# Kernel optimization log

Hardware: AMD Instinct MI355X
Metric: run time of the kernel (lower is better)

The kernel has to match this reference:

```python
import jax, jax.numpy as jnp
import numpy as np

B, S, V = 16, 512, 100000
DE, DT, DI = 100, 20, 20      # word / entity-type / entity-id embed dims
H = 128                        # lstm hidden per direction
GD = 2 * H                     # gcn_dim = 256
ITERS = 2
BANK = GD * (ITERS + 1)        # 768
N, E, P, R = 128, 48, 512, 97  # nodes, entities, h-t pairs, relations
CLS = BANK * 2 + 20            # rel_embed size with distance embedding
IN = DE + DT + DI              # encoder input size


def setup_inputs() -> dict:
    key = jax.random.key(0)
    ks = jax.random.split(key, 24)
    words = jax.random.randint(ks[0], (B, S), 0, V, dtype=jnp.int32)
    src_lengths = jax.random.randint(ks[1], (B,), S // 2, S + 1, dtype=jnp.int32)
    mask = (jnp.arange(S)[None, :] < src_lengths[:, None]).astype(jnp.int32)
    entity_type = jax.random.randint(ks[2], (B, S), 0, 7, dtype=jnp.int32)
    entity_id = jax.random.randint(ks[3], (B, S), 0, 81, dtype=jnp.int32)
    # graph_info: [start, end, entity_id, node_type]; spans inside the doc
    starts = jnp.sort(jax.random.randint(ks[4], (B, N), 0, S - 9, dtype=jnp.int32), axis=-1)
    spans = jax.random.randint(ks[5], (B, N), 1, 9, dtype=jnp.int32)
    eids = jax.random.randint(ks[6], (B, N), 0, E, dtype=jnp.int32)
    ntype = jnp.where(jnp.arange(N)[None, :] < 96, 2, 1).astype(jnp.int32) * jnp.ones((B, 1), jnp.int32)
    graph_info = jnp.stack([starts, starts + spans, eids, ntype], axis=-1)
    graph_node_num = jax.random.randint(ks[7], (B,), N // 2, N + 1, dtype=jnp.int32)
    graph_adj = jax.random.randint(ks[8], (B, N, N), 0, 5, dtype=jnp.int32)
    h_t_pairs = jax.random.randint(ks[9], (B, P, 2), 0, E, dtype=jnp.int32)
    ht_pair_distance = jax.random.randint(ks[10], (B, P), 0, 20, dtype=jnp.int32)
    sc = 0.02
    word_table = jax.random.normal(ks[11], (V, DE), jnp.float32) * sc
    word_table = word_table.at[0].set(0.0)  # padding_idx
    type_table = jax.random.normal(ks[12], (7, DT), jnp.float32) * sc
    id_table = jax.random.normal(ks[13], (81, DI), jnp.float32) * sc
    Wih_f = jax.random.normal(ks[14], (4 * H, IN), jnp.float32) * sc
    Whh_f = jax.random.normal(ks[15], (4 * H, H), jnp.float32) * sc
    b_f = jnp.zeros((4 * H,), jnp.float32)
    Wih_b = jax.random.normal(ks[16], (4 * H, IN), jnp.float32) * sc
    Whh_b = jax.random.normal(ks[17], (4 * H, H), jnp.float32) * sc
    b_b = jnp.zeros((4 * H,), jnp.float32)
    gcn_W1 = jax.random.normal(ks[18], (GD, GD), jnp.float32) * sc
    gcn_b1 = jnp.zeros((GD,), jnp.float32)
    gcn_W2 = jax.random.normal(ks[19], (GD, GD), jnp.float32) * sc
    gcn_b2 = jnp.zeros((GD,), jnp.float32)
    dis_table = jax.random.normal(ks[20], (20, 20), jnp.float32) * sc
    pW1 = jax.random.normal(ks[21], (CLS, BANK * 2), jnp.float32) * sc
    pb1 = jnp.zeros((BANK * 2,), jnp.float32)
    pW2 = jax.random.normal(ks[22], (BANK * 2, R), jnp.float32) * sc
    pb2 = jnp.zeros((R,), jnp.float32)
    return dict(words=words, mask=mask, entity_type=entity_type, entity_id=entity_id,
                src_lengths=src_lengths, graph_adj=graph_adj, graph_info=graph_info,
                graph_node_num=graph_node_num, h_t_pairs=h_t_pairs,
                ht_pair_distance=ht_pair_distance,
                word_table=word_table, type_table=type_table, id_table=id_table,
                Wih_f=Wih_f, Whh_f=Whh_f, b_f=b_f, Wih_b=Wih_b, Whh_b=Whh_b, b_b=b_b,
                gcn_W1=gcn_W1, gcn_b1=gcn_b1, gcn_W2=gcn_W2, gcn_b2=gcn_b2,
                dis_table=dis_table, pW1=pW1, pb1=pb1, pW2=pW2, pb2=pb2)


def _lstm(x, Wih, Whh, b, reverse):
    # x: [S, B, IN] -> hs: [S, B, H]
    Bsz = x.shape[1]
    h0 = jnp.zeros((Bsz, H), x.dtype)
    c0 = jnp.zeros((Bsz, H), x.dtype)
    def step(carry, xt):
        h, c = carry
        g = xt @ Wih.T + h @ Whh.T + b
        i, f, gg, o = jnp.split(g, 4, axis=-1)
        c = jax.nn.sigmoid(f) * c + jax.nn.sigmoid(i) * jnp.tanh(gg)
        h = jax.nn.sigmoid(o) * jnp.tanh(c)
        return (h, c), h
    _, hs = jax.lax.scan(step, (h0, c0), x, reverse=reverse)
    return hs


def _forward(words, mask, entity_type, entity_id, src_lengths, graph_adj, graph_info,
             graph_node_num, h_t_pairs, ht_pair_distance,
             word_table, type_table, id_table, Wih_f, Whh_f, b_f, Wih_b, Whh_b, b_b,
             gcn_W1, gcn_b1, gcn_W2, gcn_b2, dis_table, pW1, pb1, pW2, pb2):
    # --- embeddings + BiLSTM encoder ---
    src = jnp.concatenate([word_table[words], type_table[entity_type], id_table[entity_id]], axis=-1)
    xs = jnp.transpose(src, (1, 0, 2))  # [S,B,IN]
    hf = _lstm(xs, Wih_f, Whh_f, b_f, reverse=False)
    hb = _lstm(xs, Wih_b, Whh_b, b_b, reverse=True)
    enc = jnp.transpose(jnp.concatenate([hf, hb], -1), (1, 0, 2))  # [B,S,GD]
    enc = enc * mask[..., None].astype(enc.dtype)  # encoder_outputs[mask==0]=0
    # --- vectorized mergy_span_token: mean of tokens in [start,end) via cumsum ---
    cs = jnp.concatenate([jnp.zeros((enc.shape[0], 1, GD), enc.dtype), jnp.cumsum(enc, axis=1)], axis=1)
    st, en = graph_info[..., 0], graph_info[..., 1]
    span_sum = (jnp.take_along_axis(cs, en[..., None], axis=1)
                - jnp.take_along_axis(cs, st[..., None], axis=1))
    span_len = jnp.maximum(en - st, 1).astype(enc.dtype)[..., None]
    node_mask = (jnp.arange(N)[None, :] < graph_node_num[:, None])
    graph_fea = span_sum / span_len * node_mask[..., None].astype(enc.dtype)  # [B,N,GD]
    # --- GraphReasonLayer (gcn, 2 iters, dense-concat) ---
    A = ((graph_adj > 0) & node_mask[:, :, None] & node_mask[:, None, :]).astype(enc.dtype)
    Anorm = A / jnp.maximum(A.sum(-1, keepdims=True), 1.0)
    h1 = jnp.maximum(jnp.einsum('bmn,bnd->bmd', Anorm, graph_fea) @ gcn_W1 + gcn_b1, 0.0)
    h2 = jnp.maximum(jnp.einsum('bmn,bnd->bmd', Anorm, h1) @ gcn_W2 + gcn_b2, 0.0)
    feat = jnp.concatenate([graph_fea, h1, h2], axis=-1)  # [B,N,BANK]
    # --- entity bank: mean of mention nodes per entity (vectorized select matrix) ---
    m_mask = (graph_info[..., 3] == 2) & node_mask
    sel = ((graph_info[..., 2][:, None, :] == jnp.arange(E)[None, :, None]) & m_mask[:, None, :]).astype(enc.dtype)
    sel = sel / jnp.maximum(sel.sum(-1, keepdims=True), 1.0)
    entity_bank = jnp.einsum('ben,bnd->bed', sel, feat)  # [B,E,BANK]
    # --- head/tail gather + distance embedding + predict MLP ---
    h_ent = jnp.take_along_axis(entity_bank, h_t_pairs[..., 0][..., None], axis=1)
    t_ent = jnp.take_along_axis(entity_bank, h_t_pairs[..., 1][..., None], axis=1)
    rel = jnp.concatenate([h_ent, t_ent, dis_table[ht_pair_distance]], axis=-1)  # [B,P,CLS]
    scores = jnp.tanh(rel @ pW1 + pb1) @ pW2 + pb2  # [B,P,R]
    return scores


def reference(words, mask, entity_type, entity_id, src_lengths, graph_adj, graph_info,
              graph_node_num, h_t_pairs, ht_pair_distance,
              word_table, type_table, id_table, Wih_f, Whh_f, b_f, Wih_b, Whh_b, b_b,
              gcn_W1, gcn_b1, gcn_W2, gcn_b2, dis_table, pW1, pb1, pW2, pb2):
    return _forward(words, mask, entity_type, entity_id, src_lengths, graph_adj, graph_info,
                    graph_node_num, h_t_pairs, ht_pair_distance,
                    word_table, type_table, id_table, Wih_f, Whh_f, b_f, Wih_b, Whh_b, b_b,
                    gcn_W1, gcn_b1, gcn_W2, gcn_b2, dis_table, pW1, pb1, pW2, pb2)
```

## Files before the change

### kernel.cpp

```cpp
#include <hip/hip_runtime.h>
#include <math.h>

static constexpr int B_ = 16, S_ = 512, H_ = 128, G4_ = 512, IN_ = 140;
static constexpr int GD_ = 256, N_ = 128, E_ = 48, P_ = 512, R_ = 97;
static constexpr int BANK_ = 768, UC_ = 1536;

__device__ __forceinline__ float sigf(float x) { return 1.0f / (1.0f + expf(-x)); }

__global__ void transpose_w(const float* __restrict__ Wf, const float* __restrict__ Wb,
                            float* __restrict__ WfT, float* __restrict__ WbT) {
    int i = blockIdx.x * 256 + threadIdx.x;
    if (i < G4_ * IN_) {
        int j = i / IN_, k = i % IN_;
        WfT[k * G4_ + j] = Wf[i];
        WbT[k * G4_ + j] = Wb[i];
    }
}

__global__ __launch_bounds__(512) void embed_xpre(
    const int* __restrict__ words, const int* __restrict__ etype, const int* __restrict__ eidm,
    const float* __restrict__ wt, const float* __restrict__ tt, const float* __restrict__ it,
    const float* __restrict__ WfT, const float* __restrict__ WbT,
    const float* __restrict__ bf, const float* __restrict__ bb,
    float* __restrict__ xf, float* __restrict__ xb) {
    __shared__ float xl[16][IN_];
    int tid = threadIdx.x;
    int r0 = blockIdx.x * 16;
    for (int r = 0; r < 16; ++r) {
        int rid = r0 + r, s = rid >> 4, b = rid & 15;
        if (tid < IN_) {
            int k = tid; float v;
            if (k < 100)      { int w  = words[b * S_ + s]; v = wt[w * 100 + k]; }
            else if (k < 120) { int ty = etype[b * S_ + s]; v = tt[ty * 20 + (k - 100)]; }
            else              { int id = eidm[b * S_ + s];  v = it[id * 20 + (k - 120)]; }
            xl[r][k] = v;
        }
    }
    __syncthreads();
    int j = tid;
    float accf[16], accb[16];
    float bfv = bf[j], bbv = bb[j];
#pragma unroll
    for (int r = 0; r < 16; ++r) { accf[r] = bfv; accb[r] = bbv; }
#pragma unroll 4
    for (int k = 0; k < IN_; ++k) {
        float wf = WfT[k * G4_ + j], wb = WbT[k * G4_ + j];
#pragma unroll
        for (int r = 0; r < 16; ++r) {
            float x = xl[r][k];
            accf[r] += x * wf;
            accb[r] += x * wb;
        }
    }
#pragma unroll
    for (int r = 0; r < 16; ++r) {
        int rid = r0 + r;
        xf[rid * G4_ + j] = accf[r];
        xb[rid * G4_ + j] = accb[r];
    }
}

__global__ __launch_bounds__(512, 1) void lstm_kernel(
    const float* __restrict__ xf, const float* __restrict__ xb,
    const float* __restrict__ Whf, const float* __restrict__ Whb,
    float* __restrict__ hf, float* __restrict__ hb) {
    int bid = blockIdx.x;
    int dir = bid >> 4, b = bid & 15;
    const float* xpre = dir ? xb : xf;
    const float* Whh  = dir ? Whb : Whf;
    float* outp       = dir ? hb : hf;
    int tid  = threadIdx.x;
    int wave = tid >> 6;
    int lane = tid & 63;
    int j4   = lane & 15;
    int ks   = lane >> 4;
    int j    = wave * 16 + j4;

    float4 w4[4][8];
#pragma unroll
    for (int g = 0; g < 4; ++g)
#pragma unroll
        for (int q = 0; q < 8; ++q)
            w4[g][q] = *reinterpret_cast<const float4*>(
                &Whh[(j + 128 * g) * 128 + 32 * ks + 4 * q]);

    __shared__ float hsh[2][128];
    if (tid < 128) { hsh[0][tid] = 0.0f; hsh[1][tid] = 0.0f; }
    float c = 0.0f;

    int t0 = dir ? (S_ - 1) : 0;
    const float* xr0 = &xpre[(t0 * B_ + b) * G4_];
    float xi = xr0[j], xfv = xr0[j + 128], xg = xr0[j + 256], xo = xr0[j + 384];
    __syncthreads();

    for (int t = 0; t < S_; ++t) {
        int tcur = dir ? (S_ - 1 - t) : t;
        float cxi = xi, cxf = xfv, cxg = xg, cxo = xo;
        if (t < S_ - 1) {
            int tn = dir ? (S_ - 2 - t) : (t + 1);
            const float* xr = &xpre[(tn * B_ + b) * G4_];
            xi = xr[j]; xfv = xr[j + 128]; xg = xr[j + 256]; xo = xr[j + 384];
        }
        const float4* h4 = reinterpret_cast<const float4*>(&hsh[t & 1][32 * ks]);
        float ai = 0.f, af = 0.f, ag = 0.f, ao = 0.f;
#pragma unroll
        for (int q = 0; q < 8; ++q) {
            float4 hv = h4[q];
            ai += w4[0][q].x * hv.x + w4[0][q].y * hv.y + w4[0][q].z * hv.z + w4[0][q].w * hv.w;
            af += w4[1][q].x * hv.x + w4[1][q].y * hv.y + w4[1][q].z * hv.z + w4[1][q].w * hv.w;
            ag += w4[2][q].x * hv.x + w4[2][q].y * hv.y + w4[2][q].z * hv.z + w4[2][q].w * hv.w;
            ao += w4[3][q].x * hv.x + w4[3][q].y * hv.y + w4[3][q].z * hv.z + w4[3][q].w * hv.w;
        }
        ai += __shfl_xor(ai, 16); ai += __shfl_xor(ai, 32);
        af += __shfl_xor(af, 16); af += __shfl_xor(af, 32);
        ag += __shfl_xor(ag, 16); ag += __shfl_xor(ag, 32);
        ao += __shfl_xor(ao, 16); ao += __shfl_xor(ao, 32);
        ai += cxi; af += cxf; ag += cxg; ao += cxo;
        float si = sigf(ai), sf = sigf(af), so = sigf(ao);
        c = sf * c + si * tanhf(ag);
        float h = so * tanhf(c);
        if (ks == 0) {
            hsh[1 - (t & 1)][j] = h;
            outp[(tcur * B_ + b) * H_ + j] = h;
        }
        __syncthreads();
    }
}

__global__ void span_mean(const float* __restrict__ hf, const float* __restrict__ hb,
                          const int* __restrict__ ginfo, const int* __restrict__ gnum,
                          const int* __restrict__ srclen, float* __restrict__ feat) {
    int bidx = blockIdx.x, b = bidx >> 7, n = bidx & 127;
    int c = threadIdx.x;
    int st = ginfo[(b * N_ + n) * 4 + 0];
    int en = ginfo[(b * N_ + n) * 4 + 1];
    int num = gnum[b], lb = srclen[b];
    float acc = 0.0f;
    for (int s = st; s < en; ++s) {
        if (s < lb) {
            acc += (c < H_) ? hf[(s * B_ + b) * H_ + c]
                            : hb[(s * B_ + b) * H_ + (c - H_)];
        }
    }
    int len = en - st; if (len < 1) len = 1;
    float v = acc / (float)len;
    if (n >= num) v = 0.0f;
    feat[(b * N_ + n) * BANK_ + c] = v;
}

__global__ void anorm_kernel(const int* __restrict__ adj, const int* __restrict__ gnum,
                             float* __restrict__ An) {
    int bidx = blockIdx.x, b = bidx >> 7, m = bidx & 127;
    int n = threadIdx.x;
    int num = gnum[b];
    float a = (adj[(b * N_ + m) * N_ + n] > 0 && m < num && n < num) ? 1.0f : 0.0f;
    float r = a;
#pragma unroll
    for (int off = 32; off > 0; off >>= 1) r += __shfl_down(r, off, 64);
    __shared__ float wsum[2];
    if ((n & 63) == 0) wsum[n >> 6] = r;
    __syncthreads();
    float total = wsum[0] + wsum[1];
    An[(b * N_ + m) * N_ + n] = a / fmaxf(total, 1.0f);
}

__global__ void gcn_agg(const float* __restrict__ An, const float* __restrict__ feat,
                        int slice, float* __restrict__ M) {
    int b = blockIdx.x, m0 = blockIdx.y * 4;
    int tid = threadIdx.x;
    __shared__ float ar[4][N_];
    for (int e = tid; e < 4 * N_; e += 256)
        ar[e >> 7][e & 127] = An[(b * N_ + m0 + (e >> 7)) * N_ + (e & 127)];
    __syncthreads();
    float acc[4] = {0.f, 0.f, 0.f, 0.f};
    int c = tid;
    for (int n = 0; n < N_; ++n) {
        float x = feat[(b * N_ + n) * BANK_ + slice * GD_ + c];
#pragma unroll
        for (int r = 0; r < 4; ++r) acc[r] += ar[r][n] * x;
    }
#pragma unroll
    for (int r = 0; r < 4; ++r) M[(b * N_ + m0 + r) * GD_ + c] = acc[r];
}

__global__ void gcn_dense(const float* __restrict__ M, const float* __restrict__ W,
                          const float* __restrict__ bias, float* __restrict__ feat,
                          int outslice) {
    int b = blockIdx.x, m0 = blockIdx.y * 4;
    int tid = threadIdx.x;
    __shared__ float mr[4][GD_];
    for (int e = tid; e < 4 * GD_; e += 256)
        mr[e >> 8][e & 255] = M[(b * N_ + m0 + (e >> 8)) * GD_ + (e & 255)];
    __syncthreads();
    int c = tid;
    float bv = bias[c];
    float acc[4] = {bv, bv, bv, bv};
    for (int d = 0; d < GD_; ++d) {
        float wv = W[d * GD_ + c];
#pragma unroll
        for (int r = 0; r < 4; ++r) acc[r] += mr[r][d] * wv;
    }
#pragma unroll
    for (int r = 0; r < 4; ++r)
        feat[(b * N_ + m0 + r) * BANK_ + outslice * GD_ + c] = fmaxf(acc[r], 0.0f);
}

__global__ void ebank_kernel(const int* __restrict__ ginfo, const int* __restrict__ gnum,
                             const float* __restrict__ feat, float* __restrict__ eb) {
    int bidx = blockIdx.x, b = bidx / E_, e = bidx % E_;
    int tid = threadIdx.x;
    __shared__ int fl[N_];
    int num = gnum[b];
    if (tid < N_) {
        int n = tid;
        int id = ginfo[(b * N_ + n) * 4 + 2];
        int ty = ginfo[(b * N_ + n) * 4 + 3];
        fl[n] = (ty == 2 && n < num) ? id : -1;
    }
    __syncthreads();
    float a0 = 0.f, a1 = 0.f, a2 = 0.f; int cnt = 0;
    for (int n = 0; n < N_; ++n) {
        if (fl[n] == e) {
            ++cnt;
            const float* fp = &feat[(b * N_ + n) * BANK_];
            a0 += fp[tid]; a1 += fp[256 + tid]; a2 += fp[512 + tid];
        }
    }
    float inv = 1.0f / (float)(cnt > 0 ? cnt : 1);
    float* o = &eb[(b * E_ + e) * BANK_];
    o[tid] = a0 * inv; o[256 + tid] = a1 * inv; o[512 + tid] = a2 * inv;
}

__global__ void dmat_kernel(const float* __restrict__ dis, const float* __restrict__ pW1,
                            const float* __restrict__ pb1, float* __restrict__ Dm) {
    int d = blockIdx.x;
    int c = blockIdx.y * 256 + threadIdx.x;
    float acc = pb1[c];
    for (int q = 0; q < 20; ++q)
        acc += dis[d * 20 + q] * pW1[(2 * BANK_ + q) * UC_ + c];
    Dm[d * UC_ + c] = acc;
}

__global__ __launch_bounds__(256) void ugemm(const float* __restrict__ eb,
                                             const float* __restrict__ pW1,
                                             float* __restrict__ U1, float* __restrict__ U2) {
    int rt = blockIdx.x, ct = blockIdx.y;
    int tid = threadIdx.x;
    int half = (ct >= 24) ? 1 : 0;
    int jbase = (ct - half * 24) * 64;
    int wrow = half * BANK_;
    __shared__ float At[32][68];
    __shared__ float Bt[32][68];
    int rg = tid >> 4, cg = tid & 15;
    int r0 = rt * 64;
    float acc[4][4] = {};
    for (int kc = 0; kc < BANK_; kc += 32) {
#pragma unroll
        for (int i = 0; i < 8; ++i) {
            int e = tid + i * 256, r = e >> 5, k = e & 31;
            At[k][r] = eb[(r0 + r) * BANK_ + kc + k];
        }
#pragma unroll
        for (int i = 0; i < 8; ++i) {
            int e = tid + i * 256, k = e >> 6, cc = e & 63;
            Bt[k][cc] = pW1[(wrow + kc + k) * UC_ + jbase + cc];
        }
        __syncthreads();
#pragma unroll
        for (int k = 0; k < 32; ++k) {
            float4 a  = *reinterpret_cast<const float4*>(&At[k][rg * 4]);
            float4 bv = *reinterpret_cast<const float4*>(&Bt[k][cg * 4]);
            float ax[4] = {a.x, a.y, a.z, a.w};
            float bx[4] = {bv.x, bv.y, bv.z, bv.w};
#pragma unroll
            for (int r = 0; r < 4; ++r)
#pragma unroll
                for (int q = 0; q < 4; ++q) acc[r][q] += ax[r] * bx[q];
        }
        __syncthreads();
    }
    float* U = half ? U2 : U1;
#pragma unroll
    for (int r = 0; r < 4; ++r)
#pragma unroll
        for (int q = 0; q < 4; ++q)
            U[(r0 + rg * 4 + r) * UC_ + jbase + cg * 4 + q] = acc[r][q];
}

__global__ __launch_bounds__(256) void scores_kernel(
    const float* __restrict__ U1, const float* __restrict__ U2, const float* __restrict__ Dm,
    const float* __restrict__ pW2, const float* __restrict__ pb2,
    const int* __restrict__ pairs, const int* __restrict__ pdist, float* __restrict__ out) {
    int blk = blockIdx.x;
    int row0 = blk * 32;
    int b = row0 >> 9, p0 = row0 & 511;
    int tid = threadIdx.x;
    __shared__ float Tt[96 * 36];
    __shared__ float Wl[96 * 100];
    __shared__ int hidx[32], tidx[32], didx[32];
    if (tid < 32) {
        int p = p0 + tid;
        hidx[tid] = pairs[(b * P_ + p) * 2 + 0];
        tidx[tid] = pairs[(b * P_ + p) * 2 + 1];
        didx[tid] = pdist[b * P_ + p];
    }
    __syncthreads();
    int rg = tid / 25, cg = tid % 25;
    bool act = tid < 200;
    float acc[4][4] = {};
    for (int kc = 0; kc < UC_; kc += 96) {
        for (int k2 = tid; k2 < 96 * 128; k2 += 256) {
            int k = k2 >> 7, cc = k2 & 127;
            if (cc < 100) Wl[k * 100 + cc] = (cc < R_) ? pW2[(kc + k) * R_ + cc] : 0.0f;
        }
        for (int e = tid; e < 32 * 96; e += 256) {
            int r = e / 96, k = e % 96, gk = kc + k;
            float v = U1[(b * E_ + hidx[r]) * UC_ + gk]
                    + U2[(b * E_ + tidx[r]) * UC_ + gk]
                    + Dm[didx[r] * UC_ + gk];
            Tt[k * 36 + r] = tanhf(v);
        }
        __syncthreads();
        if (act) {
#pragma unroll 4
            for (int k = 0; k < 96; ++k) {
                float4 a  = *reinterpret_cast<const float4*>(&Tt[k * 36 + rg * 4]);
                float4 wv = *reinterpret_cast<const float4*>(&Wl[k * 100 + cg * 4]);
                float ax[4] = {a.x, a.y, a.z, a.w};
                float wx[4] = {wv.x, wv.y, wv.z, wv.w};
#pragma unroll
                for (int r = 0; r < 4; ++r)
#pragma unroll
                    for (int q = 0; q < 4; ++q) acc[r][q] += ax[r] * wx[q];
            }
        }
        __syncthreads();
    }
    if (act) {
#pragma unroll
        for (int r = 0; r < 4; ++r) {
            int prow = row0 + rg * 4 + r;
#pragma unroll
            for (int q = 0; q < 4; ++q) {
                int col = cg * 4 + q;
                if (col < R_) out[prow * R_ + col] = acc[r][q] + pb2[col];
            }
        }
    }
}

extern "C" void kernel_launch(void* const* d_in, const int* in_sizes, int n_in,
                              void* d_out, int out_size, void* d_ws, size_t ws_size,
                              hipStream_t stream) {
    const int*   words  = (const int*)d_in[0];
    const int*   etype  = (const int*)d_in[2];
    const int*   eidm   = (const int*)d_in[3];
    const int*   srclen = (const int*)d_in[4];
    const int*   adj    = (const int*)d_in[5];
    const int*   ginfo  = (const int*)d_in[6];
    const int*   gnum   = (const int*)d_in[7];
    const int*   pairs  = (const int*)d_in[8];
    const int*   pdist  = (const int*)d_in[9];
    const float* wt     = (const float*)d_in[10];
    const float* tt     = (const float*)d_in[11];
    const float* it     = (const float*)d_in[12];
    const float* Wihf   = (const float*)d_in[13];
    const float* Whhf   = (const float*)d_in[14];
    const float* bf     = (const float*)d_in[15];
    const float* Wihb   = (const float*)d_in[16];
    const float* Whhb   = (const float*)d_in[17];
    const float* bb     = (const float*)d_in[18];
    const float* W1     = (const float*)d_in[19];
    const float* b1     = (const float*)d_in[20];
    const float* W2     = (const float*)d_in[21];
    const float* b2     = (const float*)d_in[22];
    const float* dis    = (const float*)d_in[23];
    const float* pW1    = (const float*)d_in[24];
    const float* pb1    = (const float*)d_in[25];
    const float* pW2    = (const float*)d_in[26];
    const float* pb2    = (const float*)d_in[27];
    float* out = (float*)d_out;

    char* wsb = (char*)d_ws;
    size_t off = 0;
    auto carve = [&](size_t nf) {
        float* p = (float*)(wsb + off);
        off += ((nf * 4 + 255) / 256) * 256;
        return p;
    };
    float* WfT  = carve((size_t)IN_ * G4_);
    float* WbT  = carve((size_t)IN_ * G4_);
    float* xf   = carve((size_t)S_ * B_ * G4_);
    float* xb   = carve((size_t)S_ * B_ * G4_);
    float* hfb  = carve((size_t)S_ * B_ * H_);
    float* hbb  = carve((size_t)S_ * B_ * H_);
    float* feat = carve((size_t)B_ * N_ * BANK_);
    float* An   = carve((size_t)B_ * N_ * N_);
    float* M    = carve((size_t)B_ * N_ * GD_);
    float* eb   = carve((size_t)B_ * E_ * BANK_);
    float* U1   = carve((size_t)B_ * E_ * UC_);
    float* U2   = carve((size_t)B_ * E_ * UC_);
    float* Dm   = carve((size_t)20 * UC_);
    (void)ws_size; (void)in_sizes; (void)n_in; (void)out_size;

    transpose_w<<<(G4_ * IN_ + 255) / 256, 256, 0, stream>>>(Wihf, Wihb, WfT, WbT);
    embed_xpre<<<512, 512, 0, stream>>>(words, etype, eidm, wt, tt, it, WfT, WbT, bf, bb, xf, xb);
    lstm_kernel<<<32, 512, 0, stream>>>(xf, xb, Whhf, Whhb, hfb, hbb);
    span_mean<<<B_ * N_, 256, 0, stream>>>(hfb, hbb, ginfo, gnum, srclen, feat);
    anorm_kernel<<<B_ * N_, 128, 0, stream>>>(adj, gnum, An);
    gcn_agg<<<dim3(16, 32), 256, 0, stream>>>(An, feat, 0, M);
    gcn_dense<<<dim3(16, 32), 256, 0, stream>>>(M, W1, b1, feat, 1);
    gcn_agg<<<dim3(16, 32), 256, 0, stream>>>(An, feat, 1, M);
    gcn_dense<<<dim3(16, 32), 256, 0, stream>>>(M, W2, b2, feat, 2);
    ebank_kernel<<<B_ * E_, 256, 0, stream>>>(ginfo, gnum, feat, eb);
    dmat_kernel<<<dim3(20, 6), 256, 0, stream>>>(dis, pW1, pb1, Dm);
    ugemm<<<dim3(12, 48), 256, 0, stream>>>(eb, pW1, U1, U2);
    scores_kernel<<<256, 256, 0, stream>>>(U1, U2, Dm, pW2, pb2, pairs, pdist, out);
}
```

Measured before the change: 1.334 ms.

## Merge prep kernels, use fast transcendental approximations, pad LDS and vectorize inner loops

Three small setup kernels (weight transpose, adjacency normalisation, distance matrix) are folded into one launch to cut launch overhead. The LSTM recurrence and the scores kernel switch to fast exp/rcp-based sigmoid and tanh, and the LSTM's shared hidden-state buffer is padded to avoid bank conflicts. The embedding staging is transposed so inputs load as float4, and the GCN loops are unrolled by four with float4 LDS reads. The fast math approximations trade some accuracy in the recurrent path for shorter per-step latency.

```diff
diff --git a/kernel.cpp b/kernel.cpp
--- a/kernel.cpp
+++ b/kernel.cpp
@@ -5,15 +5,50 @@
 static constexpr int GD_ = 256, N_ = 128, E_ = 48, P_ = 512, R_ = 97;
 static constexpr int BANK_ = 768, UC_ = 1536;
 
-__device__ __forceinline__ float sigf(float x) { return 1.0f / (1.0f + expf(-x)); }
-
-__global__ void transpose_w(const float* __restrict__ Wf, const float* __restrict__ Wb,
-                            float* __restrict__ WfT, float* __restrict__ WbT) {
-    int i = blockIdx.x * 256 + threadIdx.x;
-    if (i < G4_ * IN_) {
-        int j = i / IN_, k = i % IN_;
-        WfT[k * G4_ + j] = Wf[i];
-        WbT[k * G4_ + j] = Wb[i];
+__device__ __forceinline__ float fsig(float x) {
+    return __builtin_amdgcn_rcpf(1.0f + __expf(-x));
+}
+__device__ __forceinline__ float ftanh(float x) {
+    float e = __expf(2.0f * fminf(x, 15.0f));
+    return (e - 1.0f) * __builtin_amdgcn_rcpf(e + 1.0f);
+}
+
+__global__ __launch_bounds__(256) void misc_prep(
+    const float* __restrict__ Wf, const float* __restrict__ Wb,
+    float* __restrict__ WfT, float* __restrict__ WbT,
+    const int* __restrict__ adj, const int* __restrict__ gnum, float* __restrict__ An,
+    const float* __restrict__ dis, const float* __restrict__ pW1,
+    const float* __restrict__ pb1, float* __restrict__ Dm) {
+    int bid = blockIdx.x, tid = threadIdx.x;
+    if (bid < 280) {
+        int i = bid * 256 + tid;
+        if (i < G4_ * IN_) {
+            int jj = i / IN_, k = i - jj * IN_;
+            WfT[k * G4_ + jj] = Wf[i];
+            WbT[k * G4_ + jj] = Wb[i];
+        }
+    } else if (bid < 1304) {
+        int rr = (bid - 280) * 2 + (tid >> 7);
+        int b = rr >> 7, m = rr & 127, n = tid & 127;
+        int num = gnum[b];
+        float a = (adj[(b * N_ + m) * N_ + n] > 0 && m < num && n < num) ? 1.0f : 0.0f;
+        float r = a;
+#pragma unroll
+        for (int off = 32; off > 0; off >>= 1) r += __shfl_down(r, off, 64);
+        __shared__ float ws4[4];
+        if ((tid & 63) == 0) ws4[tid >> 6] = r;
+        __syncthreads();
+        int w0 = (tid >> 7) * 2;
+        float total = ws4[w0] + ws4[w0 + 1];
+        An[(b * N_ + m) * N_ + n] = a / fmaxf(total, 1.0f);
+    } else {
+        int e = bid - 1304;
+        int d = e / 6, cch = e - d * 6;
+        int ci = cch * 256 + tid;
+        float acc = pb1[ci];
+#pragma unroll 4
+        for (int q = 0; q < 20; ++q) acc += dis[d * 20 + q] * pW1[(2 * BANK_ + q) * UC_ + ci];
+        Dm[d * UC_ + ci] = acc;
     }
 }
 
@@ -23,18 +58,17 @@
     const float* __restrict__ WfT, const float* __restrict__ WbT,
     const float* __restrict__ bf, const float* __restrict__ bb,
     float* __restrict__ xf, float* __restrict__ xb) {
-    __shared__ float xl[16][IN_];
+    __shared__ float xl[IN_][20];
     int tid = threadIdx.x;
     int r0 = blockIdx.x * 16;
-    for (int r = 0; r < 16; ++r) {
+    for (int e = tid; e < 16 * IN_; e += 512) {
+        int r = e / IN_, k = e - r * IN_;
         int rid = r0 + r, s = rid >> 4, b = rid & 15;
-        if (tid < IN_) {
-            int k = tid; float v;
-            if (k < 100)      { int w  = words[b * S_ + s]; v = wt[w * 100 + k]; }
-            else if (k < 120) { int ty = etype[b * S_ + s]; v = tt[ty * 20 + (k - 100)]; }
-            else              { int id = eidm[b * S_ + s];  v = it[id * 20 + (k - 120)]; }
-            xl[r][k] = v;
-        }
+        float v;
+        if (k < 100)      v = wt[words[b * S_ + s] * 100 + k];
+        else if (k < 120) v = tt[etype[b * S_ + s] * 20 + (k - 100)];
+        else              v = it[eidm[b * S_ + s] * 20 + (k - 120)];
+        xl[k][r] = v;
     }
     __syncthreads();
     int j = tid;
@@ -42,14 +76,19 @@
     float bfv = bf[j], bbv = bb[j];
 #pragma unroll
     for (int r = 0; r < 16; ++r) { accf[r] = bfv; accb[r] = bbv; }
-#pragma unroll 4
+#pragma unroll 2
     for (int k = 0; k < IN_; ++k) {
         float wf = WfT[k * G4_ + j], wb = WbT[k * G4_ + j];
+        float4 x0 = *reinterpret_cast<const float4*>(&xl[k][0]);
+        float4 x1 = *reinterpret_cast<const float4*>(&xl[k][4]);
+        float4 x2 = *reinterpret_cast<const float4*>(&xl[k][8]);
+        float4 x3 = *reinterpret_cast<const float4*>(&xl[k][12]);
+        float xr[16] = {x0.x, x0.y, x0.z, x0.w, x1.x, x1.y, x1.z, x1.w,
+                        x2.x, x2.y, x2.z, x2.w, x3.x, x3.y, x3.z, x3.w};
 #pragma unroll
         for (int r = 0; r < 16; ++r) {
-            float x = xl[r][k];
-            accf[r] += x * wf;
-            accb[r] += x * wb;
+            accf[r] += xr[r] * wf;
+            accb[r] += xr[r] * wb;
         }
     }
 #pragma unroll
@@ -60,15 +99,15 @@
     }
 }
 
-__global__ __launch_bounds__(512, 1) void lstm_kernel(
+__global__ __launch_bounds__(512, 2) void lstm_kernel(
     const float* __restrict__ xf, const float* __restrict__ xb,
-    const float* __restrict__ Whf, const float* __restrict__ Whb,
-    float* __restrict__ hf, float* __restrict__ hb) {
+    const float* Whf, const float* Whb,
+    float* hfo, float* hbo) {
     int bid = blockIdx.x;
     int dir = bid >> 4, b = bid & 15;
     const float* xpre = dir ? xb : xf;
     const float* Whh  = dir ? Whb : Whf;
-    float* outp       = dir ? hb : hf;
+    float* outp       = dir ? hbo : hfo;
     int tid  = threadIdx.x;
     int wave = tid >> 6;
     int lane = tid & 63;
@@ -84,8 +123,11 @@
             w4[g][q] = *reinterpret_cast<const float4*>(
                 &Whh[(j + 128 * g) * 128 + 32 * ks + 4 * q]);
 
-    __shared__ float hsh[2][128];
-    if (tid < 128) { hsh[0][tid] = 0.0f; hsh[1][tid] = 0.0f; }
+    __shared__ float hsh[2][4 * 36];
+    if (tid < 128) {
+        hsh[0][(tid >> 5) * 36 + (tid & 31)] = 0.0f;
+        hsh[1][(tid >> 5) * 36 + (tid & 31)] = 0.0f;
+    }
     float c = 0.0f;
 
     int t0 = dir ? (S_ - 1) : 0;
@@ -101,11 +143,11 @@
             const float* xr = &xpre[(tn * B_ + b) * G4_];
             xi = xr[j]; xfv = xr[j + 128]; xg = xr[j + 256]; xo = xr[j + 384];
         }
-        const float4* h4 = reinterpret_cast<const float4*>(&hsh[t & 1][32 * ks]);
+        const float* hrow = &hsh[t & 1][ks * 36];
         float ai = 0.f, af = 0.f, ag = 0.f, ao = 0.f;
 #pragma unroll
         for (int q = 0; q < 8; ++q) {
-            float4 hv = h4[q];
+            float4 hv = *reinterpret_cast<const float4*>(&hrow[4 * q]);
             ai += w4[0][q].x * hv.x + w4[0][q].y * hv.y + w4[0][q].z * hv.z + w4[0][q].w * hv.w;
             af += w4[1][q].x * hv.x + w4[1][q].y * hv.y + w4[1][q].z * hv.z + w4[1][q].w * hv.w;
             ag += w4[2][q].x * hv.x + w4[2][q].y * hv.y + w4[2][q].z * hv.z + w4[2][q].w * hv.w;
@@ -116,11 +158,11 @@
         ag += __shfl_xor(ag, 16); ag += __shfl_xor(ag, 32);
         ao += __shfl_xor(ao, 16); ao += __shfl_xor(ao, 32);
         ai += cxi; af += cxf; ag += cxg; ao += cxo;
-        float si = sigf(ai), sf = sigf(af), so = sigf(ao);
-        c = sf * c + si * tanhf(ag);
-        float h = so * tanhf(c);
+        float si = fsig(ai), sf = fsig(af), so = fsig(ao);
+        c = sf * c + si * ftanh(ag);
+        float h = so * ftanh(c);
         if (ks == 0) {
-            hsh[1 - (t & 1)][j] = h;
+            hsh[1 - (t & 1)][(j >> 5) * 36 + (j & 31)] = h;
             outp[(tcur * B_ + b) * H_ + j] = h;
         }
         __syncthreads();
@@ -148,22 +190,6 @@
     feat[(b * N_ + n) * BANK_ + c] = v;
 }
 
-__global__ void anorm_kernel(const int* __restrict__ adj, const int* __restrict__ gnum,
-                             float* __restrict__ An) {
-    int bidx = blockIdx.x, b = bidx >> 7, m = bidx & 127;
-    int n = threadIdx.x;
-    int num = gnum[b];
-    float a = (adj[(b * N_ + m) * N_ + n] > 0 && m < num && n < num) ? 1.0f : 0.0f;
-    float r = a;
-#pragma unroll
-    for (int off = 32; off > 0; off >>= 1) r += __shfl_down(r, off, 64);
-    __shared__ float wsum[2];
-    if ((n & 63) == 0) wsum[n >> 6] = r;
-    __syncthreads();
-    float total = wsum[0] + wsum[1];
-    An[(b * N_ + m) * N_ + n] = a / fmaxf(total, 1.0f);
-}
-
 __global__ void gcn_agg(const float* __restrict__ An, const float* __restrict__ feat,
                         int slice, float* __restrict__ M) {
     int b = blockIdx.x, m0 = blockIdx.y * 4;
@@ -174,10 +200,17 @@
     __syncthreads();
     float acc[4] = {0.f, 0.f, 0.f, 0.f};
     int c = tid;
-    for (int n = 0; n < N_; ++n) {
-        float x = feat[(b * N_ + n) * BANK_ + slice * GD_ + c];
-#pragma unroll
-        for (int r = 0; r < 4; ++r) acc[r] += ar[r][n] * x;
+    const float* fbase = &feat[(size_t)b * N_ * BANK_ + slice * GD_ + c];
+    for (int n = 0; n < N_; n += 4) {
+        float x0 = fbase[(size_t)(n + 0) * BANK_];
+        float x1 = fbase[(size_t)(n + 1) * BANK_];
+        float x2 = fbase[(size_t)(n + 2) * BANK_];
+        float x3 = fbase[(size_t)(n + 3) * BANK_];
+#pragma unroll
+        for (int r = 0; r < 4; ++r) {
+            float4 a = *reinterpret_cast<const float4*>(&ar[r][n]);
+            acc[r] += a.x * x0 + a.y * x1 + a.z * x2 + a.w * x3;
+        }
     }
 #pragma unroll
     for (int r = 0; r < 4; ++r) M[(b * N_ + m0 + r) * GD_ + c] = acc[r];
@@ -195,10 +228,16 @@
     int c = tid;
     float bv = bias[c];
     float acc[4] = {bv, bv, bv, bv};
-    for (int d = 0; d < GD_; ++d) {
-        float wv = W[d * GD_ + c];
-#pragma unroll
-        for (int r = 0; r < 4; ++r) acc[r] += mr[r][d] * wv;
+    for (int d = 0; d < GD_; d += 4) {
+        float w0 = W[(d + 0) * GD_ + c];
+        float w1 = W[(d + 1) * GD_ + c];
+        float w2 = W[(d + 2) * GD_ + c];
+        float w3 = W[(d + 3) * GD_ + c];
+#pragma unroll
+        for (int r = 0; r < 4; ++r) {
+            float4 m = *reinterpret_cast<const float4*>(&mr[r][d]);
+            acc[r] += m.x * w0 + m.y * w1 + m.z * w2 + m.w * w3;
+        }
     }
 #pragma unroll
     for (int r = 0; r < 4; ++r)
@@ -229,16 +268,6 @@
     float inv = 1.0f / (float)(cnt > 0 ? cnt : 1);
     float* o = &eb[(b * E_ + e) * BANK_];
     o[tid] = a0 * inv; o[256 + tid] = a1 * inv; o[512 + tid] = a2 * inv;
-}
-
-__global__ void dmat_kernel(const float* __restrict__ dis, const float* __restrict__ pW1,
-                            const float* __restrict__ pb1, float* __restrict__ Dm) {
-    int d = blockIdx.x;
-    int c = blockIdx.y * 256 + threadIdx.x;
-    float acc = pb1[c];
-    for (int q = 0; q < 20; ++q)
-        acc += dis[d * 20 + q] * pW1[(2 * BANK_ + q) * UC_ + c];
-    Dm[d * UC_ + c] = acc;
 }
 
 __global__ __launch_bounds__(256) void ugemm(const float* __restrict__ eb,
@@ -318,7 +347,7 @@
             float v = U1[(b * E_ + hidx[r]) * UC_ + gk]
                     + U2[(b * E_ + tidx[r]) * UC_ + gk]
                     + Dm[didx[r] * UC_ + gk];
-            Tt[k * 36 + r] = tanhf(v);
+            Tt[k * 36 + r] = ftanh(v);
         }
         __syncthreads();
         if (act) {
@@ -403,17 +432,15 @@
     float* Dm   = carve((size_t)20 * UC_);
     (void)ws_size; (void)in_sizes; (void)n_in; (void)out_size;
 
-    transpose_w<<<(G4_ * IN_ + 255) / 256, 256, 0, stream>>>(Wihf, Wihb, WfT, WbT);
+    misc_prep<<<1424, 256, 0, stream>>>(Wihf, Wihb, WfT, WbT, adj, gnum, An, dis, pW1, pb1, Dm);
     embed_xpre<<<512, 512, 0, stream>>>(words, etype, eidm, wt, tt, it, WfT, WbT, bf, bb, xf, xb);
     lstm_kernel<<<32, 512, 0, stream>>>(xf, xb, Whhf, Whhb, hfb, hbb);
     span_mean<<<B_ * N_, 256, 0, stream>>>(hfb, hbb, ginfo, gnum, srclen, feat);
-    anorm_kernel<<<B_ * N_, 128, 0, stream>>>(adj, gnum, An);
     gcn_agg<<<dim3(16, 32), 256, 0, stream>>>(An, feat, 0, M);
     gcn_dense<<<dim3(16, 32), 256, 0, stream>>>(M, W1, b1, feat, 1);
     gcn_agg<<<dim3(16, 32), 256, 0, stream>>>(An, feat, 1, M);
     gcn_dense<<<dim3(16, 32), 256, 0, stream>>>(M, W2, b2, feat, 2);
     ebank_kernel<<<B_ * E_, 256, 0, stream>>>(ginfo, gnum, feat, eb);
-    dmat_kernel<<<dim3(20, 6), 256, 0, stream>>>(dis, pW1, pb1, Dm);
     ugemm<<<dim3(12, 48), 256, 0, stream>>>(eb, pW1, U1, U2);
     scores_kernel<<<256, 256, 0, stream>>>(U1, U2, Dm, pW2, pb2, pairs, pdist, out);
 }
```

After: 1.101 ms. 1.21x faster.
